# Kernel optimization log

Hardware: AMD Instinct MI355X
Metric: run time of the kernel (lower is better)

Reference implementation:

```python
import jax, jax.numpy as jnp
import numpy as np

N_ART = 50000
N_COMM = 50000
F_IN = 768
PROJ = 1024
HID = 256
OUT = 128


def _sage(x_src, x_dst, ei, Wl, bl, Wr):
    # PyG SAGEConv (aggr='mean', root_weight=True): lin_l(mean_j x_j) + lin_r(x_dst)
    src, dst = ei[0], ei[1]
    n_dst = x_dst.shape[0]
    msg = x_src[src]                                   # [E, d_src] gather
    agg = jax.ops.segment_sum(msg, dst, num_segments=n_dst)
    cnt = jax.ops.segment_sum(jnp.ones((ei.shape[1],), x_src.dtype), dst, num_segments=n_dst)
    mean = agg / jnp.maximum(cnt, 1.0)[:, None]
    return mean @ Wl + bl + x_dst @ Wr


def setup_inputs() -> dict:
    key = jax.random.key(0)
    ks = jax.random.split(key, 22)
    w = lambda k, s: (jax.random.normal(k, s, jnp.float32) * 0.02)
    inp = {
        "article_x": jax.random.normal(ks[0], (N_ART, F_IN), jnp.float32),
        "community_x": jax.random.normal(ks[1], (N_COMM, F_IN), jnp.float32),
        "e_wb": jax.random.randint(ks[2], (2, 200000), 0, N_COMM, jnp.int32),
        "e_mb": jax.random.randint(ks[3], (2, 200000), 0, N_COMM, jnp.int32),
        "e_int": jax.random.randint(ks[4], (2, 500000), 0, N_COMM, jnp.int32),
        # lin1 / lin2 projections (F_IN -> PROJ)
        "W1": w(ks[5], (F_IN, PROJ)), "b1": jnp.zeros((PROJ,), jnp.float32),
        "W2": w(ks[6], (F_IN, PROJ)), "b2": jnp.zeros((PROJ,), jnp.float32),
        # conv1: src dim PROJ, dst dim PROJ -> HID
        "Wl1": w(ks[7], (PROJ, HID)), "bl1": jnp.zeros((HID,), jnp.float32), "Wr1": w(ks[8], (PROJ, HID)),
        # conv2: src dim PROJ, dst dim HID -> HID
        "Wl2": w(ks[9], (PROJ, HID)), "bl2": jnp.zeros((HID,), jnp.float32), "Wr2": w(ks[10], (HID, HID)),
        # conv3: src dim HID, dst dim F_IN (raw community.x) -> HID
        "Wl3": w(ks[11], (HID, HID)), "bl3": jnp.zeros((HID,), jnp.float32), "Wr3": w(ks[12], (F_IN, HID)),
        # lin3: HID -> OUT
        "W3": w(ks[13], (HID, OUT)), "b3": jnp.zeros((OUT,), jnp.float32),
    }
    return inp


def reference(article_x, community_x, e_wb, e_mb, e_int,
              W1, b1, W2, b2,
              Wl1, bl1, Wr1, Wl2, bl2, Wr2, Wl3, bl3, Wr3,
              W3, b3):
    ax = article_x @ W1 + b1          # [N_art, PROJ]
    cx = community_x @ W2 + b2        # [N_comm, PROJ]
    h1 = jax.nn.relu(_sage(ax, cx, e_wb, Wl1, bl1, Wr1))            # [N_comm, HID]
    h2 = jax.nn.relu(_sage(ax, h1, e_mb, Wl2, bl2, Wr2))            # [N_comm, HID]
    h3 = jax.nn.relu(_sage(h2, community_x, e_int, Wl3, bl3, Wr3))  # [N_comm, HID]
    return h3 @ W3 + b3               # [N_comm, OUT]
```

## Files before the change

### kernel.cpp

```cpp
#include <hip/hip_runtime.h>
#include <hip/hip_bf16.h>

#define N_NODES 50000
#define M_PAD   50048
#define MT_     391
#define F_IN    768
#define PROJ    1024
#define HID     256
#define OUTD    128
#define E_WB    200000
#define E_MB    200000
#define E_INT   500000
#define BIGM    (1 << 30)

typedef float f32x4 __attribute__((ext_vector_type(4)));
typedef __bf16 bf16x8 __attribute__((ext_vector_type(8)));

__device__ __forceinline__ float bf2f(unsigned short u) {
  union { unsigned int i; float f; } x; x.i = ((unsigned int)u) << 16; return x.f;
}
__device__ __forceinline__ unsigned short f2bf(float f) {
  union { float f; unsigned int i; } x; x.f = f;
  unsigned int r = x.i + 0x7fff + ((x.i >> 16) & 1);
  return (unsigned short)(r >> 16);
}

__device__ __forceinline__ void gl_lds16(const void* g, void* l) {
  __builtin_amdgcn_global_load_lds((const __attribute__((address_space(1))) void*)g,
                                   (__attribute__((address_space(3))) void*)l, 16, 0, 0);
}

__device__ __forceinline__ void dev_cast8(const float* __restrict__ src,
                                          unsigned short* __restrict__ dst, int blk) {
  int i = blk * 256 + threadIdx.x;
  const float4* s4 = (const float4*)src;
  float4 a = s4[(long long)i * 2], b = s4[(long long)i * 2 + 1];
  uint4 o;
  o.x = (unsigned int)f2bf(a.x) | ((unsigned int)f2bf(a.y) << 16);
  o.y = (unsigned int)f2bf(a.z) | ((unsigned int)f2bf(a.w) << 16);
  o.z = (unsigned int)f2bf(b.x) | ((unsigned int)f2bf(b.y) << 16);
  o.w = (unsigned int)f2bf(b.z) | ((unsigned int)f2bf(b.w) << 16);
  ((uint4*)dst)[i] = o;
}

__device__ __forceinline__ void dev_tcast(const float* __restrict__ src,
                                          unsigned short* __restrict__ dst,
                                          int R, int C, int blk, float (*tile)[33]) {
  int bx = blk % (C / 32), by = blk / (C / 32);
  int tx = threadIdx.x & 31, ty = threadIdx.x >> 5;
  int x = bx * 32 + tx, y0 = by * 32;
  for (int i = ty; i < 32; i += 8) tile[i][tx] = src[(long long)(y0 + i) * C + x];
  __syncthreads();
  int xo = by * 32 + tx, yo0 = bx * 32;
  for (int i = ty; i < 32; i += 8) dst[(long long)(yo0 + i) * R + xo] = f2bf(tile[tx][i]);
}

__global__ void prep_all_kernel(const float* __restrict__ W1, const float* __restrict__ W2,
                                const float* __restrict__ Wl1, const float* __restrict__ Wl2,
                                const float* __restrict__ Wr1, const float* __restrict__ Wr2,
                                const float* __restrict__ Wl3, const float* __restrict__ Wr3,
                                const float* __restrict__ W3,
                                const float* __restrict__ b1, const float* __restrict__ b2,
                                const float* __restrict__ bl1,
                                unsigned short* __restrict__ W1bf, unsigned short* __restrict__ W2bf,
                                unsigned short* __restrict__ WlT, unsigned short* __restrict__ Wr1T,
                                unsigned short* __restrict__ GT_wr3, unsigned short* __restrict__ Wr2T,
                                unsigned short* __restrict__ Wl3T, unsigned short* __restrict__ W3T,
                                float* __restrict__ gb1, float* __restrict__ gb2,
                                float* __restrict__ bv1) {
  __shared__ float tile[32][33];
  int b = blockIdx.x;
  if (b < 384) { dev_cast8(W1, W1bf, b); return; }
  b -= 384;
  if (b < 384) { dev_cast8(W2, W2bf, b); return; }
  b -= 384;
  if (b < 256) { dev_tcast(Wl1, WlT, PROJ, HID, b, tile); return; }
  b -= 256;
  if (b < 256) { dev_tcast(Wl2, WlT + 256 * PROJ, PROJ, HID, b, tile); return; }
  b -= 256;
  if (b < 256) { dev_tcast(Wr1, Wr1T, PROJ, HID, b, tile); return; }
  b -= 256;
  if (b < 192) { dev_tcast(Wr3, GT_wr3, F_IN, HID, b, tile); return; }
  b -= 192;
  if (b < 64) { dev_tcast(Wr2, Wr2T, HID, HID, b, tile); return; }
  b -= 64;
  if (b < 64) { dev_tcast(Wl3, Wl3T, HID, HID, b, tile); return; }
  b -= 64;
  if (b < 32) { dev_tcast(W3, W3T, HID, OUTD, b, tile); return; }
  b -= 32;
  int j = threadIdx.x;
  int out = b >> 3, pg = b & 7;
  const float* vb = (out == 2) ? b2 : b1;
  const float* W = (out == 0) ? Wl1 : (out == 1 ? Wl2 : Wr1);
  float s = 0.f;
  int p0 = pg * 128;
#pragma unroll 4
  for (int p = p0; p < p0 + 128; ++p) s += vb[p] * W[p * HID + j];
  if (out == 2 && pg == 0) s += bl1[j];
  float* dst = (out == 0) ? gb1 : (out == 1 ? gb2 : bv1);
  atomicAdd(&dst[j], s);
}

__global__ void cast_nodes_kernel(const float* __restrict__ ax, const float* __restrict__ cx,
                                  unsigned short* __restrict__ dst) {
  int i = blockIdx.x * 256 + threadIdx.x;
  int row = i / 96, c8 = i % 96;
  const float* src = ax;
  int vrow = row;
  if (row >= M_PAD) { src = cx; vrow = row - M_PAD; }
  uint4 o;
  if (vrow < N_NODES) {
    const float4* s4 = (const float4*)src;
    long long base = (long long)vrow * 192 + c8 * 2;
    float4 a = s4[base], bq = s4[base + 1];
    o.x = (unsigned int)f2bf(a.x) | ((unsigned int)f2bf(a.y) << 16);
    o.y = (unsigned int)f2bf(a.z) | ((unsigned int)f2bf(a.w) << 16);
    o.z = (unsigned int)f2bf(bq.x) | ((unsigned int)f2bf(bq.y) << 16);
    o.w = (unsigned int)f2bf(bq.z) | ((unsigned int)f2bf(bq.w) << 16);
  } else {
    o.x = o.y = o.z = o.w = 0u;
  }
  ((uint4*)dst)[i] = o;
}

__global__ void count_all_kernel(const int* __restrict__ dwb, const int* __restrict__ dmb,
                                 const int* __restrict__ dint,
                                 int* __restrict__ cwb, int* __restrict__ cmb,
                                 int* __restrict__ cint) {
  int i = blockIdx.x * blockDim.x + threadIdx.x;
  const int total = E_WB + E_MB + E_INT;
  if (i >= total) return;
  if (i < E_WB) atomicAdd(&cwb[dwb[i]], 1);
  else if (i < E_WB + E_MB) atomicAdd(&cmb[dmb[i - E_WB]], 1);
  else atomicAdd(&cint[dint[i - E_WB - E_MB]], 1);
}

__global__ void scan3_kernel(const int* __restrict__ c0, const int* __restrict__ c1,
                             const int* __restrict__ c2,
                             int* __restrict__ o0, int* __restrict__ o1, int* __restrict__ o2) {
  const int* cnt = blockIdx.x == 0 ? c0 : (blockIdx.x == 1 ? c1 : c2);
  int* off = blockIdx.x == 0 ? o0 : (blockIdx.x == 1 ? o1 : o2);
  const int n = N_NODES;
  __shared__ int part[1024];
  int t = threadIdx.x;
  const int chunk = (n + 1023) / 1024;
  int lo = t * chunk, hi = lo + chunk; if (hi > n) hi = n; if (lo > n) lo = n;
  int s = 0;
  for (int i = lo; i < hi; ++i) s += cnt[i];
  part[t] = s; __syncthreads();
  for (int d = 1; d < 1024; d <<= 1) {
    int v = part[t];
    if (t >= d) v += part[t - d];
    __syncthreads();
    part[t] = v;
    __syncthreads();
  }
  int run = (t == 0) ? 0 : part[t - 1];
  for (int i = lo; i < hi; ++i) { off[i] = run; run += cnt[i]; }
  if (t == 1023) off[n] = part[1023];
}

__global__ void fill_all_kernel(const int* __restrict__ ewb, const int* __restrict__ emb,
                                const int* __restrict__ eint,
                                const int* __restrict__ owb, const int* __restrict__ omb,
                                const int* __restrict__ oint,
                                int* __restrict__ curwb, int* __restrict__ curmb,
                                int* __restrict__ curint,
                                int* __restrict__ swb, int* __restrict__ smb,
                                int* __restrict__ sint) {
  int i = blockIdx.x * blockDim.x + threadIdx.x;
  const int total = E_WB + E_MB + E_INT;
  if (i >= total) return;
  if (i < E_WB) {
    int s = ewb[i], d = ewb[E_WB + i];
    int p = atomicAdd(&curwb[d], 1);
    swb[owb[d] + p] = s;
  } else if (i < E_WB + E_MB) {
    int e = i - E_WB;
    int s = emb[e], d = emb[E_MB + e];
    int p = atomicAdd(&curmb[d], 1);
    smb[omb[d] + p] = s;
  } else {
    int e = i - E_WB - E_MB;
    int s = eint[e], d = eint[E_INT + e];
    int p = atomicAdd(&curint[d], 1);
    sint[oint[d] + p] = s;
  }
}

template <int EPI>
__global__ void __launch_bounds__(256, 2)
gemm_bt_kernel(const unsigned short* __restrict__ A, const unsigned short* __restrict__ BT0,
               const unsigned short* __restrict__ BT1, int mt_split,
               void* __restrict__ Cv, int K, int N, int Mhalf, int Mvalid,
               const float* __restrict__ bias, const unsigned short* __restrict__ addm,
               int addm_stride) {
  __shared__ __align__(16) unsigned short lA[2 * 4096];
  __shared__ __align__(16) unsigned short lB[2 * 4096];
  const int tid = threadIdx.x;
  const int lane = tid & 63;
  const int wave = tid >> 6;
  const int NT = N >> 7;
  const int mt = blockIdx.x / NT;
  const int nt = blockIdx.x % NT;
  const int m0 = mt * 128, n0 = nt * 128;
  const int wm = (wave & 1) * 64, wn = (wave >> 1) * 64;
  const unsigned short* BT = (mt < mt_split) ? BT0 : BT1;

  f32x4 acc[4][4];
#pragma unroll
  for (int i = 0; i < 4; ++i)
#pragma unroll
    for (int j = 0; j < 4; ++j)
#pragma unroll
      for (int r = 0; r < 4; ++r) acc[i][j][r] = 0.f;

  const int r0 = tid >> 2;
  const int c0 = (tid & 3) * 8;
  const uint4* A4 = (const uint4*)A;
  const uint4* B4 = (const uint4*)BT;
  const int K8 = K >> 3;
  const int mrow = lane & 15, kq = lane >> 4;

  for (int kt = 0; kt < K; kt += 64) {
    __syncthreads();
#pragma unroll
    for (int s = 0; s < 2; ++s) {
      const int kc = (kt + s * 32 + c0) >> 3;
      unsigned short* lAw = &lA[s * 4096 + wave * 512];
      unsigned short* lBw = &lB[s * 4096 + wave * 512];
      gl_lds16(&A4[(long long)(m0 + r0) * K8 + kc], lAw);
      gl_lds16(&A4[(long long)(m0 + 64 + r0) * K8 + kc], lAw + 2048);
      gl_lds16(&B4[(long long)(n0 + r0) * K8 + kc], lBw);
      gl_lds16(&B4[(long long)(n0 + 64 + r0) * K8 + kc], lBw + 2048);
    }
    __syncthreads();
#pragma unroll
    for (int s = 0; s < 2; ++s) {
      bf16x8 af[4], bfr[4];
#pragma unroll
      for (int i = 0; i < 4; ++i)
        af[i] = *(const bf16x8*)&lA[s * 4096 + (wm + i * 16 + mrow) * 32 + kq * 8];
#pragma unroll
      for (int j = 0; j < 4; ++j)
        bfr[j] = *(const bf16x8*)&lB[s * 4096 + (wn + j * 16 + mrow) * 32 + kq * 8];
#pragma unroll
      for (int i = 0; i < 4; ++i)
#pragma unroll
        for (int j = 0; j < 4; ++j)
          acc[i][j] = __builtin_amdgcn_mfma_f32_16x16x32_bf16(af[i], bfr[j], acc[i][j], 0, 0, 0);
    }
  }

  const int col_l = lane & 15, rq = lane >> 4;
#pragma unroll
  for (int i = 0; i < 4; ++i) {
#pragma unroll
    for (int j = 0; j < 4; ++j) {
#pragma unroll
      for (int r = 0; r < 4; ++r) {
        int R = m0 + wm + i * 16 + rq * 4 + r;
        int Cc = n0 + wn + j * 16 + col_l;
        int vr = (R >= Mhalf) ? R - Mhalf : R;
        if (vr < Mvalid) {
          float v = acc[i][j][r];
          if constexpr (EPI == 0) {
            ((unsigned short*)Cv)[(long long)R * N + Cc] = f2bf(v);
          } else if constexpr (EPI == 1) {
            v += bias[Cc] + bf2f(addm[(long long)R * addm_stride + Cc]);
            v = v > 0.f ? v : 0.f;
            ((unsigned short*)Cv)[(long long)R * N + Cc] = f2bf(v);
          } else {
            ((float*)Cv)[(long long)R * N + Cc] = v + bias[Cc];
          }
        }
      }
    }
  }
}

template <int MODE>
__global__ void agg_kernel(const unsigned short* __restrict__ S, int s_stride,
                           const int* __restrict__ off, const int* __restrict__ srcl,
                           const float* __restrict__ gb, const float* __restrict__ bvec,
                           const unsigned short* __restrict__ addm, int a_stride,
                           unsigned short* __restrict__ out) {
  int d = blockIdx.x * 4 + (threadIdx.x >> 6);
  int c = (threadIdx.x & 63) * 4;
  if (d >= N_NODES) {
    ushort4 z; z.x = z.y = z.z = z.w = 0;
    *(ushort4*)&out[(long long)d * HID + c] = z;
    return;
  }
  int lo = off[d], hi = off[d + 1];
  float s0 = 0.f, s1 = 0.f, s2 = 0.f, s3 = 0.f;
  for (int i = lo; i < hi; ++i) {
    int sidx = srcl[i];
    uint2 v = *(const uint2*)&S[(long long)sidx * s_stride + c];
    s0 += bf2f((unsigned short)(v.x & 0xffff));
    s1 += bf2f((unsigned short)(v.x >> 16));
    s2 += bf2f((unsigned short)(v.y & 0xffff));
    s3 += bf2f((unsigned short)(v.y >> 16));
  }
  int deg = hi - lo;
  float inv = deg > 0 ? 1.f / (float)deg : 0.f;
  float v0 = s0 * inv, v1 = s1 * inv, v2 = s2 * inv, v3 = s3 * inv;
  if constexpr (MODE != 2) {
    float g = deg > 0 ? 1.f : 0.f;
    uint2 am = *(const uint2*)&addm[(long long)d * a_stride + c];
    v0 += g * gb[c] + bvec[c] + bf2f((unsigned short)(am.x & 0xffff));
    v1 += g * gb[c + 1] + bvec[c + 1] + bf2f((unsigned short)(am.x >> 16));
    v2 += g * gb[c + 2] + bvec[c + 2] + bf2f((unsigned short)(am.y & 0xffff));
    v3 += g * gb[c + 3] + bvec[c + 3] + bf2f((unsigned short)(am.y >> 16));
    v0 = fmaxf(v0, 0.f); v1 = fmaxf(v1, 0.f); v2 = fmaxf(v2, 0.f); v3 = fmaxf(v3, 0.f);
  }
  ushort4 o;
  o.x = f2bf(v0); o.y = f2bf(v1); o.z = f2bf(v2); o.w = f2bf(v3);
  *(ushort4*)&out[(long long)d * HID + c] = o;
}

extern "C" void kernel_launch(void* const* d_in, const int* in_sizes, int n_in,
                              void* d_out, int out_size, void* d_ws, size_t ws_size,
                              hipStream_t stream) {
  const float* article_x = (const float*)d_in[0];
  const float* community_x = (const float*)d_in[1];
  const int* e_wb = (const int*)d_in[2];
  const int* e_mb = (const int*)d_in[3];
  const int* e_int = (const int*)d_in[4];
  const float* W1 = (const float*)d_in[5];
  const float* b1 = (const float*)d_in[6];
  const float* W2 = (const float*)d_in[7];
  const float* b2 = (const float*)d_in[8];
  const float* Wl1 = (const float*)d_in[9];
  const float* bl1 = (const float*)d_in[10];
  const float* Wr1 = (const float*)d_in[11];
  const float* Wl2 = (const float*)d_in[12];
  const float* bl2 = (const float*)d_in[13];
  const float* Wr2 = (const float*)d_in[14];
  const float* Wl3 = (const float*)d_in[15];
  const float* bl3 = (const float*)d_in[16];
  const float* Wr3 = (const float*)d_in[17];
  const float* W3 = (const float*)d_in[18];
  const float* b3 = (const float*)d_in[19];

  char* base = (char*)d_ws;
  size_t off = 0;
  auto alloc = [&](size_t bytes) -> void* {
    void* r = base + off;
    off += (bytes + 255) & ~(size_t)255;
    return r;
  };

  unsigned short* Xs = (unsigned short*)alloc((size_t)2 * M_PAD * F_IN * 2);
  unsigned short* AP = (unsigned short*)alloc((size_t)2 * M_PAD * 512 * 2);
  unsigned short* CR = AP + (size_t)M_PAD * 512;
  unsigned short* h1bf = (unsigned short*)alloc((size_t)M_PAD * HID * 2);
  unsigned short* HR2 = (unsigned short*)alloc((size_t)M_PAD * HID * 2);
  unsigned short* h2bf = (unsigned short*)alloc((size_t)M_PAD * HID * 2);
  unsigned short* mean3bf = (unsigned short*)alloc((size_t)M_PAD * HID * 2);
  unsigned short* h3bf = (unsigned short*)alloc((size_t)M_PAD * HID * 2);
  unsigned short* W1bf = (unsigned short*)alloc((size_t)F_IN * PROJ * 2);
  unsigned short* W2bf = (unsigned short*)alloc((size_t)F_IN * PROJ * 2);
  unsigned short* WlT = (unsigned short*)alloc((size_t)512 * PROJ * 2);
  unsigned short* Wr1T = (unsigned short*)alloc((size_t)HID * PROJ * 2);
  unsigned short* F12T = (unsigned short*)alloc((size_t)512 * F_IN * 2);
  unsigned short* GT = (unsigned short*)alloc((size_t)512 * F_IN * 2);
  unsigned short* Wr2T = (unsigned short*)alloc((size_t)HID * HID * 2);
  unsigned short* Wl3T = (unsigned short*)alloc((size_t)HID * HID * 2);
  unsigned short* W3T = (unsigned short*)alloc((size_t)OUTD * HID * 2);
  int* ints_base = (int*)alloc((size_t)6 * N_NODES * 4);
  float* gb1 = (float*)alloc(HID * 4);
  float* gb2 = (float*)alloc(HID * 4);
  float* bv1 = (float*)alloc(HID * 4);
  int* cnt_wb = ints_base;
  int* cur_wb = ints_base + N_NODES;
  int* cnt_mb = ints_base + 2 * N_NODES;
  int* cur_mb = ints_base + 3 * N_NODES;
  int* cnt_int = ints_base + 4 * N_NODES;
  int* cur_int = ints_base + 5 * N_NODES;
  int* off_wb = (int*)alloc((size_t)(N_NODES + 1) * 4);
  int* off_mb = (int*)alloc((size_t)(N_NODES + 1) * 4);
  int* off_int = (int*)alloc((size_t)(N_NODES + 1) * 4);
  int* srcl_wb = (int*)alloc((size_t)E_WB * 4);
  int* srcl_mb = (int*)alloc((size_t)E_MB * 4);
  int* srcl_int = (int*)alloc((size_t)E_INT * 4);

  size_t zbytes = (size_t)((char*)bv1 + HID * 4 - (char*)ints_base);
  hipMemsetAsync(ints_base, 0, zbytes, stream);

  prep_all_kernel<<<1912, 256, 0, stream>>>(W1, W2, Wl1, Wl2, Wr1, Wr2, Wl3, Wr3, W3,
                                            b1, b2, bl1,
                                            W1bf, W2bf, WlT, Wr1T, GT + 256 * F_IN,
                                            Wr2T, Wl3T, W3T, gb1, gb2, bv1);

  cast_nodes_kernel<<<2 * M_PAD * 96 / 256, 256, 0, stream>>>(article_x, community_x, Xs);

  const int etot = E_WB + E_MB + E_INT;
  count_all_kernel<<<(etot + 255) / 256, 256, 0, stream>>>(e_wb + E_WB, e_mb + E_MB, e_int + E_INT,
                                                           cnt_wb, cnt_mb, cnt_int);
  scan3_kernel<<<3, 1024, 0, stream>>>(cnt_wb, cnt_mb, cnt_int, off_wb, off_mb, off_int);
  fill_all_kernel<<<(etot + 255) / 256, 256, 0, stream>>>(e_wb, e_mb, e_int, off_wb, off_mb, off_int,
                                                          cur_wb, cur_mb, cur_int,
                                                          srcl_wb, srcl_mb, srcl_int);

  gemm_bt_kernel<0><<<6 * 6, 256, 0, stream>>>(WlT, W1bf, W2bf, 4, F12T, PROJ, F_IN,
                                               BIGM, F_IN, nullptr, nullptr, 0);

  gemm_bt_kernel<0><<<2 * MT_ * 4, 256, 0, stream>>>(Xs, F12T, GT, MT_, AP, F_IN, 512,
                                                     M_PAD, N_NODES, nullptr, nullptr, 0);

  agg_kernel<0><<<M_PAD / 4, 256, 0, stream>>>(AP, 512, off_wb, srcl_wb, gb1, bv1, CR, 512, h1bf);

  gemm_bt_kernel<0><<<MT_ * 2, 256, 0, stream>>>(h1bf, Wr2T, nullptr, BIGM, HR2, HID, HID,
                                                 BIGM, N_NODES, nullptr, nullptr, 0);
  agg_kernel<1><<<M_PAD / 4, 256, 0, stream>>>(AP + 256, 512, off_mb, srcl_mb, gb2, bl2, HR2, 256, h2bf);

  agg_kernel<2><<<M_PAD / 4, 256, 0, stream>>>(h2bf, 256, off_int, srcl_int, nullptr, nullptr,
                                               nullptr, 0, mean3bf);
  gemm_bt_kernel<1><<<MT_ * 2, 256, 0, stream>>>(mean3bf, Wl3T, nullptr, BIGM, h3bf, HID, HID,
                                                 BIGM, N_NODES, bl3, CR + 256, 512);

  gemm_bt_kernel<2><<<MT_, 256, 0, stream>>>(h3bf, W3T, nullptr, BIGM, d_out, HID, OUTD,
                                             BIGM, N_NODES, b3, nullptr, 0);

  (void)in_sizes; (void)n_in; (void)out_size; (void)ws_size;
}
```

Measured before the change: 908.5 us.

## Swizzle GEMM LDS layout, group tile order by M, raise occupancy bound

The bf16 MFMA GEMM now XOR-swizzles the 16-byte k-chunks in LDS by row, so fragment reads from shared memory avoid bank conflicts. Blocks are remapped so groups of 8 consecutive M-tiles share each N-tile, which improves L2 reuse of B and A tiles. The launch bound is raised from 2 to 4 blocks per SM, which may force register spills given the 64-float accumulator.

```diff
diff --git a/kernel.cpp b/kernel.cpp
--- a/kernel.cpp
+++ b/kernel.cpp
@@ -189,7 +189,7 @@
 }
 
 template <int EPI>
-__global__ void __launch_bounds__(256, 2)
+__global__ void __launch_bounds__(256, 4)
 gemm_bt_kernel(const unsigned short* __restrict__ A, const unsigned short* __restrict__ BT0,
                const unsigned short* __restrict__ BT1, int mt_split,
                void* __restrict__ Cv, int K, int N, int Mhalf, int Mvalid,
@@ -201,8 +201,21 @@
   const int lane = tid & 63;
   const int wave = tid >> 6;
   const int NT = N >> 7;
-  const int mt = blockIdx.x / NT;
-  const int nt = blockIdx.x % NT;
+
+  int mt, nt;
+  {
+    const int G = NT << 3;
+    const int main_count = ((int)gridDim.x / G) * G;
+    if ((int)blockIdx.x < main_count) {
+      int j = blockIdx.x >> 3;
+      mt = (j / NT) * 8 + (blockIdx.x & 7);
+      nt = j % NT;
+    } else {
+      int idx = blockIdx.x - main_count;
+      mt = (main_count / G) * 8 + idx / NT;
+      nt = idx % NT;
+    }
+  }
   const int m0 = mt * 128, n0 = nt * 128;
   const int wm = (wave & 1) * 64, wn = (wave >> 1) * 64;
   const unsigned short* BT = (mt < mt_split) ? BT0 : BT1;
@@ -216,7 +229,7 @@
       for (int r = 0; r < 4; ++r) acc[i][j][r] = 0.f;
 
   const int r0 = tid >> 2;
-  const int c0 = (tid & 3) * 8;
+  const int c0 = (((tid & 3) ^ ((tid >> 3) & 3)) * 8);
   const uint4* A4 = (const uint4*)A;
   const uint4* B4 = (const uint4*)BT;
   const int K8 = K >> 3;
@@ -239,11 +252,15 @@
     for (int s = 0; s < 2; ++s) {
       bf16x8 af[4], bfr[4];
 #pragma unroll
-      for (int i = 0; i < 4; ++i)
-        af[i] = *(const bf16x8*)&lA[s * 4096 + (wm + i * 16 + mrow) * 32 + kq * 8];
-#pragma unroll
-      for (int j = 0; j < 4; ++j)
-        bfr[j] = *(const bf16x8*)&lB[s * 4096 + (wn + j * 16 + mrow) * 32 + kq * 8];
+      for (int i = 0; i < 4; ++i) {
+        int Ra = wm + i * 16 + mrow;
+        af[i] = *(const bf16x8*)&lA[s * 4096 + Ra * 32 + ((kq ^ ((Ra >> 1) & 3)) * 8)];
+      }
+#pragma unroll
+      for (int j = 0; j < 4; ++j) {
+        int Rb = wn + j * 16 + mrow;
+        bfr[j] = *(const bf16x8*)&lB[s * 4096 + Rb * 32 + ((kq ^ ((Rb >> 1) & 3)) * 8)];
+      }
 #pragma unroll
       for (int i = 0; i < 4; ++i)
 #pragma unroll
```

Measured after the change: 886.7 us. -2.4%, faster.
